# Kernel tuning notes

Measured on AMD Instinct MI355X. Metric: run time of the kernel, lower is better.

The kernel has to match this reference:

```python
import jax, jax.numpy as jnp
import numpy as np

_EPS_COS = 1e-8  # F.cosine_similarity default eps
_EPS_ADD = 1e-12


def setup_inputs() -> dict:
    key = jax.random.key(0)
    ks = jax.random.split(key, 7)
    B, N, M, INT_SHIFT = 256, 4096, 64, 3
    return {
        "beta": jax.random.uniform(ks[0], (B, 1), dtype=jnp.float32),
        "kappa": jax.random.normal(ks[1], (B, M), dtype=jnp.float32),
        "gamma": jax.random.uniform(ks[2], (B, 1), dtype=jnp.float32),
        "g": jax.random.uniform(ks[3], (B, 1), dtype=jnp.float32),
        "s": jax.random.uniform(ks[4], (B, INT_SHIFT), dtype=jnp.float32),
        "w_prev": jax.random.uniform(ks[5], (B, N), dtype=jnp.float32),
        "memory": jax.random.normal(ks[6], (B, N, M), dtype=jnp.float32),
        "int_shift": INT_SHIFT,
    }


def reference(beta, kappa, gamma, g, s, w_prev, memory, int_shift):
    # --- content addressing: cosine similarity + softmax over N ---
    a = memory + _EPS_ADD                      # [B, N, M]
    b = kappa[:, None, :] + _EPS_ADD           # [B, 1, M]
    dot = jnp.einsum("bnm,bqm->bn", a, b)
    na = jnp.sqrt(jnp.sum(a * a, axis=-1))     # [B, N]
    nb = jnp.sqrt(jnp.sum(b * b, axis=-1))     # [B, 1]
    sim = dot / (jnp.maximum(na, _EPS_COS) * jnp.maximum(nb, _EPS_COS))
    w_c = jax.nn.softmax(beta * sim, axis=1)   # [B, N]

    # --- interpolate with previous weighting ---
    w_g = g * w_c + (1.0 - g) * w_prev         # [B, N]

    # --- circular shift: result[b, i] = sum_j s[b, j] * w_g[b, (i + j - 1) mod N]
    # (equivalent to the per-batch padded conv1d in the original, batched via roll)
    w_hat = jnp.zeros_like(w_g)
    for j in range(int_shift):
        w_hat = w_hat + s[:, j:j + 1] * jnp.roll(w_g, 1 - j, axis=1)

    # --- sharpen ---
    w = w_hat ** gamma
    w = w / (jnp.sum(w, axis=1, keepdims=True) + _EPS_ADD)
    return w
```

## Files before the change

kernel.cpp:

```cpp
#include <hip/hip_runtime.h>
#include <math.h>

#define EPS_COS 1e-8f
#define EPS_ADD 1e-12f

typedef float f4 __attribute__((ext_vector_type(4)));


constexpr int NTHREADS = 1024;
constexpr int NWAVES   = NTHREADS / 64;
constexpr int MAX_N    = 4096;

__global__ __launch_bounds__(NTHREADS, 1) void ntm_fused_kernel(
    const float* __restrict__ beta,
    const float* __restrict__ kappa,
    const float* __restrict__ gamma,
    const float* __restrict__ g,
    const float* __restrict__ s,
    const float* __restrict__ w_prev,
    const float* __restrict__ mem,
    float* __restrict__ out,
    int N, int S)
{
    const int b    = blockIdx.x;
    const int tid  = threadIdx.x;
    const int lane = tid & 63;
    const int wave = tid >> 6;
    const int l16  = lane & 15;
    const int rg   = lane >> 4;

    __shared__ float sh[MAX_N];
    __shared__ float red[NWAVES];

    const f4 wp_reg = reinterpret_cast<const f4*>(w_prev + (size_t)b * N)[tid];

    f4 kv = reinterpret_cast<const f4*>(kappa + (size_t)b * 64)[l16];
    kv += (f4)EPS_ADD;
    float nb2 = kv.x * kv.x + kv.y * kv.y + kv.z * kv.z + kv.w * kv.w;
#pragma unroll
    for (int m = 1; m < 16; m <<= 1) nb2 += __shfl_xor(nb2, m);
    const float bscale = beta[b] / fmaxf(sqrtf(nb2), EPS_COS);

    const int nRound = N >> 6;
    const int row0   = wave * 4 + rg;
    const f4* p = reinterpret_cast<const f4*>(mem + (size_t)b * N * 64)
                  + (size_t)row0 * 16 + l16;

    f4 a0 = p[0], a1 = p[1024], a2 = p[2048], a3 = p[3072];
    float lsum = 0.0f;

    for (int it = 0; it < nRound; it += 4) {
        const f4 c0 = a0, c1 = a1, c2 = a2, c3 = a3;
        if (it + 4 < nRound) {
            const f4* pn = p + (size_t)(it + 4) * 1024;
            a0 = pn[0]; a1 = pn[1024]; a2 = pn[2048]; a3 = pn[3072];
        }
#pragma unroll
        for (int u = 0; u < 4; ++u) {
            const f4 v = (u == 0) ? c0 : (u == 1) ? c1 : (u == 2) ? c2 : c3;
            float d  = v.x * kv.x + v.y * kv.y + v.z * kv.z + v.w * kv.w;
            float n2 = v.x * v.x + v.y * v.y + v.z * v.z + v.w * v.w;
#pragma unroll
            for (int m = 1; m < 16; m <<= 1) {
                d  += __shfl_xor(d, m);
                n2 += __shfl_xor(n2, m);
            }
            const float t = bscale * d * rsqrtf(fmaxf(n2, 1e-16f));
            const float e = expf(t);
            if (l16 == 0) {
                sh[row0 + (it + u) * 64] = e;
                lsum += e;
            }
        }
    }

#pragma unroll
    for (int m = 1; m < 64; m <<= 1) lsum += __shfl_xor(lsum, m);
    if (lane == 0) red[wave] = lsum;
    __syncthreads();
    float tot = 0.0f;
#pragma unroll
    for (int i = 0; i < NWAVES; ++i) tot += red[i];

    const float gv = g[b];
    const float ws = gv / tot;
    f4* sh4 = reinterpret_cast<f4*>(sh);
    {
        const f4 ev = sh4[tid];
        sh4[tid] = ws * ev + (1.0f - gv) * wp_reg;
    }
    __syncthreads();

    const float gam = gamma[b];
    float sv[8];
    const int Sc = (S < 8) ? S : 8;
    for (int j = 0; j < Sc; ++j) sv[j] = s[(size_t)b * S + j];

    const int i0 = tid * 4;
    const int mask = N - 1;
    float o[4];
    float ssum = 0.0f;
#pragma unroll
    for (int k = 0; k < 4; ++k) {
        float wh = 0.0f;
        for (int j = 0; j < Sc; ++j) {
            const int idx = (i0 + k + j - 1) & mask;
            wh += sv[j] * sh[idx];
        }
        o[k] = powf(wh, gam);
        ssum += o[k];
    }

#pragma unroll
    for (int m = 1; m < 64; m <<= 1) ssum += __shfl_xor(ssum, m);
    if (lane == 0) red[wave] = ssum;
    __syncthreads();
    float stot = 0.0f;
#pragma unroll
    for (int i = 0; i < NWAVES; ++i) stot += red[i];

    const float inv_den = 1.0f / (stot + EPS_ADD);
    f4 ov;
    ov.x = o[0] * inv_den; ov.y = o[1] * inv_den;
    ov.z = o[2] * inv_den; ov.w = o[3] * inv_den;
    reinterpret_cast<f4*>(out + (size_t)b * N)[tid] = ov;
}

extern "C" void kernel_launch(void* const* d_in, const int* in_sizes, int n_in,
                              void* d_out, int out_size, void* d_ws, size_t ws_size,
                              hipStream_t stream) {
    const float* beta   = (const float*)d_in[0];
    const float* kappa  = (const float*)d_in[1];
    const float* gamma  = (const float*)d_in[2];
    const float* g      = (const float*)d_in[3];
    const float* s      = (const float*)d_in[4];
    const float* w_prev = (const float*)d_in[5];
    const float* mem    = (const float*)d_in[6];
    float* out          = (float*)d_out;

    const int B = in_sizes[0];
    const int N = in_sizes[5] / B;
    const int S = in_sizes[4] / B;

    ntm_fused_kernel<<<B, NTHREADS, 0, stream>>>(
        beta, kappa, gamma, g, s, w_prev, mem, out, N, S);
}
```

Baseline: 54.23 us.

## Use DPP row reductions and double-buffered contiguous memory loads

Measured after the change: 54.00 us. Within noise of the previous version (-0.4%).

```diff
diff --git a/kernel.cpp b/kernel.cpp
--- a/kernel.cpp
+++ b/kernel.cpp
@@ -10,6 +10,19 @@
 constexpr int NTHREADS = 1024;
 constexpr int NWAVES   = NTHREADS / 64;
 constexpr int MAX_N    = 4096;
+
+__device__ __forceinline__ float row_sum16_lane0(float x) {
+    int t;
+    t = __builtin_amdgcn_update_dpp(0, __float_as_int(x), 0x108, 0xf, 0xf, true);
+    x += __int_as_float(t);
+    t = __builtin_amdgcn_update_dpp(0, __float_as_int(x), 0x104, 0xf, 0xf, true);
+    x += __int_as_float(t);
+    t = __builtin_amdgcn_update_dpp(0, __float_as_int(x), 0x102, 0xf, 0xf, true);
+    x += __int_as_float(t);
+    t = __builtin_amdgcn_update_dpp(0, __float_as_int(x), 0x101, 0xf, 0xf, true);
+    x += __int_as_float(t);
+    return x;
+}
 
 __global__ __launch_bounds__(NTHREADS, 1) void ntm_fused_kernel(
     const float* __restrict__ beta,
@@ -37,39 +50,69 @@
     f4 kv = reinterpret_cast<const f4*>(kappa + (size_t)b * 64)[l16];
     kv += (f4)EPS_ADD;
     float nb2 = kv.x * kv.x + kv.y * kv.y + kv.z * kv.z + kv.w * kv.w;
-#pragma unroll
-    for (int m = 1; m < 16; m <<= 1) nb2 += __shfl_xor(nb2, m);
+    nb2 = row_sum16_lane0(nb2);
+    nb2 = __shfl(nb2, (lane >> 4) << 4);
     const float bscale = beta[b] / fmaxf(sqrtf(nb2), EPS_COS);
 
-    const int nRound = N >> 6;
-    const int row0   = wave * 4 + rg;
+    const int nIter = N >> 8;
+    const int rowb  = wave * 16 + rg;
     const f4* p = reinterpret_cast<const f4*>(mem + (size_t)b * N * 64)
-                  + (size_t)row0 * 16 + l16;
+                  + (size_t)wave * 256 + lane;
 
-    f4 a0 = p[0], a1 = p[1024], a2 = p[2048], a3 = p[3072];
     float lsum = 0.0f;
+    f4 aA[4], aB[4];
+#pragma unroll
+    for (int u = 0; u < 4; ++u) aA[u] = p[u * 64];
+#pragma unroll
+    for (int u = 0; u < 4; ++u) aB[u] = p[4096 + u * 64];
 
-    for (int it = 0; it < nRound; it += 4) {
-        const f4 c0 = a0, c1 = a1, c2 = a2, c3 = a3;
-        if (it + 4 < nRound) {
-            const f4* pn = p + (size_t)(it + 4) * 1024;
-            a0 = pn[0]; a1 = pn[1024]; a2 = pn[2048]; a3 = pn[3072];
+    for (int it = 0; it < nIter; it += 2) {
+        {
+            f4 c[4];
+#pragma unroll
+            for (int u = 0; u < 4; ++u) c[u] = aA[u];
+            if (it + 2 < nIter) {
+                const f4* pn = p + (size_t)(it + 2) * 4096;
+#pragma unroll
+                for (int u = 0; u < 4; ++u) aA[u] = pn[u * 64];
+            }
+#pragma unroll
+            for (int u = 0; u < 4; ++u) {
+                const f4 v = c[u];
+                float d  = v.x * kv.x + v.y * kv.y + v.z * kv.z + v.w * kv.w;
+                float n2 = v.x * v.x + v.y * v.y + v.z * v.z + v.w * v.w;
+                d  = row_sum16_lane0(d);
+                n2 = row_sum16_lane0(n2);
+                if (l16 == 0) {
+                    const float t = bscale * d * rsqrtf(fmaxf(n2, 1e-16f));
+                    const float e = expf(t);
+                    sh[rowb + u * 4 + it * 256] = e;
+                    lsum += e;
+                }
+            }
         }
+        {
+            f4 c[4];
 #pragma unroll
-        for (int u = 0; u < 4; ++u) {
-            const f4 v = (u == 0) ? c0 : (u == 1) ? c1 : (u == 2) ? c2 : c3;
-            float d  = v.x * kv.x + v.y * kv.y + v.z * kv.z + v.w * kv.w;
-            float n2 = v.x * v.x + v.y * v.y + v.z * v.z + v.w * v.w;
+            for (int u = 0; u < 4; ++u) c[u] = aB[u];
+            if (it + 3 < nIter) {
+                const f4* pn = p + (size_t)(it + 3) * 4096;
 #pragma unroll
-            for (int m = 1; m < 16; m <<= 1) {
-                d  += __shfl_xor(d, m);
-                n2 += __shfl_xor(n2, m);
+                for (int u = 0; u < 4; ++u) aB[u] = pn[u * 64];
             }
-            const float t = bscale * d * rsqrtf(fmaxf(n2, 1e-16f));
-            const float e = expf(t);
-            if (l16 == 0) {
-                sh[row0 + (it + u) * 64] = e;
-                lsum += e;
+#pragma unroll
+            for (int u = 0; u < 4; ++u) {
+                const f4 v = c[u];
+                float d  = v.x * kv.x + v.y * kv.y + v.z * kv.z + v.w * kv.w;
+                float n2 = v.x * v.x + v.y * v.y + v.z * v.z + v.w * v.w;
+                d  = row_sum16_lane0(d);
+                n2 = row_sum16_lane0(n2);
+                if (l16 == 0) {
+                    const float t = bscale * d * rsqrtf(fmaxf(n2, 1e-16f));
+                    const float e = expf(t);
+                    sh[rowb + u * 4 + (it + 1) * 256] = e;
+                    lsum += e;
+                }
             }
         }
     }
```

## Deepen memory prefetch, use DPP row reductions, and nontemporal loads

Applied to the files above, without the earlier changes.

After: 55.08 us. Within noise of the previous version (+1.6%).

```diff
diff --git a/kernel.cpp b/kernel.cpp
--- a/kernel.cpp
+++ b/kernel.cpp
@@ -10,6 +10,19 @@
 constexpr int NTHREADS = 1024;
 constexpr int NWAVES   = NTHREADS / 64;
 constexpr int MAX_N    = 4096;
+
+__device__ __forceinline__ float row_sum16_lane0(float x) {
+    int t;
+    t = __builtin_amdgcn_update_dpp(0, __float_as_int(x), 0x108, 0xf, 0xf, true);
+    x += __int_as_float(t);
+    t = __builtin_amdgcn_update_dpp(0, __float_as_int(x), 0x104, 0xf, 0xf, true);
+    x += __int_as_float(t);
+    t = __builtin_amdgcn_update_dpp(0, __float_as_int(x), 0x102, 0xf, 0xf, true);
+    x += __int_as_float(t);
+    t = __builtin_amdgcn_update_dpp(0, __float_as_int(x), 0x101, 0xf, 0xf, true);
+    x += __int_as_float(t);
+    return x;
+}
 
 __global__ __launch_bounds__(NTHREADS, 1) void ntm_fused_kernel(
     const float* __restrict__ beta,
@@ -37,42 +50,60 @@
     f4 kv = reinterpret_cast<const f4*>(kappa + (size_t)b * 64)[l16];
     kv += (f4)EPS_ADD;
     float nb2 = kv.x * kv.x + kv.y * kv.y + kv.z * kv.z + kv.w * kv.w;
-#pragma unroll
-    for (int m = 1; m < 16; m <<= 1) nb2 += __shfl_xor(nb2, m);
+    nb2 = row_sum16_lane0(nb2);
+    nb2 = __shfl(nb2, (lane >> 4) << 4);
     const float bscale = beta[b] / fmaxf(sqrtf(nb2), EPS_COS);
 
-    const int nRound = N >> 6;
-    const int row0   = wave * 4 + rg;
+    const int nIter = N >> 8;
+    const int rowb  = wave * 16 + rg;
     const f4* p = reinterpret_cast<const f4*>(mem + (size_t)b * N * 64)
-                  + (size_t)row0 * 16 + l16;
+                  + (size_t)wave * 256 + lane;
 
-    f4 a0 = p[0], a1 = p[1024], a2 = p[2048], a3 = p[3072];
     float lsum = 0.0f;
+    f4 aA[4], aB[4], aC[4], aD[4];
+#pragma unroll
+    for (int u = 0; u < 4; ++u) aA[u] = __builtin_nontemporal_load(p + u * 64);
+#pragma unroll
+    for (int u = 0; u < 4; ++u) aB[u] = __builtin_nontemporal_load(p + 4096 + u * 64);
+#pragma unroll
+    for (int u = 0; u < 4; ++u) aC[u] = __builtin_nontemporal_load(p + 8192 + u * 64);
+#pragma unroll
+    for (int u = 0; u < 4; ++u) aD[u] = __builtin_nontemporal_load(p + 12288 + u * 64);
 
-    for (int it = 0; it < nRound; it += 4) {
-        const f4 c0 = a0, c1 = a1, c2 = a2, c3 = a3;
-        if (it + 4 < nRound) {
-            const f4* pn = p + (size_t)(it + 4) * 1024;
-            a0 = pn[0]; a1 = pn[1024]; a2 = pn[2048]; a3 = pn[3072];
-        }
-#pragma unroll
-        for (int u = 0; u < 4; ++u) {
-            const f4 v = (u == 0) ? c0 : (u == 1) ? c1 : (u == 2) ? c2 : c3;
-            float d  = v.x * kv.x + v.y * kv.y + v.z * kv.z + v.w * kv.w;
-            float n2 = v.x * v.x + v.y * v.y + v.z * v.z + v.w * v.w;
-#pragma unroll
-            for (int m = 1; m < 16; m <<= 1) {
-                d  += __shfl_xor(d, m);
-                n2 += __shfl_xor(n2, m);
-            }
-            const float t = bscale * d * rsqrtf(fmaxf(n2, 1e-16f));
-            const float e = expf(t);
-            if (l16 == 0) {
-                sh[row0 + (it + u) * 64] = e;
-                lsum += e;
-            }
-        }
+#define NTM_BODY(BUF, IT_OFF)                                                   \
+    {                                                                           \
+        f4 c[4];                                                                \
+        _Pragma("unroll")                                                       \
+        for (int u = 0; u < 4; ++u) c[u] = BUF[u];                              \
+        if (it + (IT_OFF) + 4 < nIter) {                                        \
+            const f4* pn = p + (size_t)(it + (IT_OFF) + 4) * 4096;              \
+            _Pragma("unroll")                                                   \
+            for (int u = 0; u < 4; ++u)                                         \
+                BUF[u] = __builtin_nontemporal_load(pn + u * 64);               \
+        }                                                                       \
+        _Pragma("unroll")                                                       \
+        for (int u = 0; u < 4; ++u) {                                           \
+            const f4 v = c[u];                                                  \
+            float d  = v.x * kv.x + v.y * kv.y + v.z * kv.z + v.w * kv.w;       \
+            float n2 = v.x * v.x + v.y * v.y + v.z * v.z + v.w * v.w;           \
+            d  = row_sum16_lane0(d);                                            \
+            n2 = row_sum16_lane0(n2);                                           \
+            if (l16 == 0) {                                                     \
+                const float t = bscale * d * rsqrtf(fmaxf(n2, 1e-16f));         \
+                const float e = expf(t);                                        \
+                sh[rowb + u * 4 + (it + (IT_OFF)) * 256] = e;                    \
+                lsum += e;                                                      \
+            }                                                                   \
+        }                                                                       \
     }
+
+    for (int it = 0; it < nIter; it += 4) {
+        NTM_BODY(aA, 0)
+        NTM_BODY(aB, 1)
+        NTM_BODY(aC, 2)
+        NTM_BODY(aD, 3)
+    }
+#undef NTM_BODY
 
 #pragma unroll
     for (int m = 1; m < 64; m <<= 1) lsum += __shfl_xor(lsum, m);
```
